# Performance work log

Hardware: AMD Instinct MI355X
Metric: run time of the kernel (lower is better)

## Reference

```python
import jax, jax.numpy as jnp
import numpy as np

D = 128          # embed_dim
N = 400000       # rows in each source state buffer (h_bot/c_bot and h_buf/c_buf)
K = 200000       # gathers per source per child side (M = 2*K merge targets)


def setup_inputs() -> dict:
    key = jax.random.key(0)
    ks = jax.random.split(key, 10)
    h_bot = jax.random.normal(ks[0], (N, D), dtype=jnp.float32)
    c_bot = jax.random.normal(ks[1], (N, D), dtype=jnp.float32)
    h_buf = jax.random.normal(ks[2], (N, D), dtype=jnp.float32)
    c_buf = jax.random.normal(ks[3], (N, D), dtype=jnp.float32)
    bot_from_l = jax.random.randint(ks[4], (K,), 0, N, dtype=jnp.int32)
    prev_from_l = jax.random.randint(ks[5], (K,), 0, N, dtype=jnp.int32)
    bot_from_r = jax.random.randint(ks[6], (K,), 0, N, dtype=jnp.int32)
    prev_from_r = jax.random.randint(ks[7], (K,), 0, N, dtype=jnp.int32)
    # BinaryTreeLSTMCell params: 5 gates (i, o, u, f_l, f_r) over [h_l; h_r]
    W = jax.random.normal(ks[8], (2 * D, 5 * D), dtype=jnp.float32) * (1.0 / np.sqrt(2 * D))
    b = jnp.zeros((5 * D,), dtype=jnp.float32)
    return {"h_bot": h_bot, "c_bot": c_bot, "h_buf": h_buf, "c_buf": c_buf,
            "bot_from_l": bot_from_l, "prev_from_l": prev_from_l,
            "bot_from_r": bot_from_r, "prev_from_r": prev_from_r,
            "W": W, "b": b}


def _multi_select(bot_src, prev_src, bot_from, prev_from):
    # multi_index_select with 'to' ids in concat order: gather rows from the two
    # source buffers into the [M, D] merge-target buffer.
    return jnp.concatenate([bot_src[bot_from], prev_src[prev_from]], axis=0)


def _binary_tree_lstm_cell(h_l, c_l, h_r, c_r, W, b):
    # N-ary (N=2) TreeLSTM merge cell, no input x.
    gates = jnp.concatenate([h_l, h_r], axis=1) @ W + b  # [M, 5D]
    i, o, u, f_l, f_r = jnp.split(gates, 5, axis=1)
    c = jax.nn.sigmoid(i) * jnp.tanh(u) \
        + jax.nn.sigmoid(f_l) * c_l + jax.nn.sigmoid(f_r) * c_r
    h = jax.nn.sigmoid(o) * jnp.tanh(c)
    return h, c


def reference(h_bot, c_bot, h_buf, c_buf,
              bot_from_l, prev_from_l, bot_from_r, prev_from_r, W, b):
    # batch_tree_lstm2: tree_state_select gathers for left and right children,
    # then one BinaryTreeLSTMCell merge over all M targets.
    h_l = _multi_select(h_bot, h_buf, bot_from_l, prev_from_l)
    c_l = _multi_select(c_bot, c_buf, bot_from_l, prev_from_l)
    h_r = _multi_select(h_bot, h_buf, bot_from_r, prev_from_r)
    c_r = _multi_select(c_bot, c_buf, bot_from_r, prev_from_r)
    h, c = _binary_tree_lstm_cell(h_l, c_l, h_r, c_r, W, b)
    return jnp.stack([h, c])  # [2, M, D]
```

## Files before the change

### kernel.cpp

```cpp
#include <hip/hip_runtime.h>

typedef __attribute__((ext_vector_type(8))) short short8_t;
typedef __attribute__((ext_vector_type(4))) float f32x4_t;

#define DDIM 128
#define BM   32
#define LDA  264

__device__ __forceinline__ unsigned short f2bf(float x) {
  union { float f; unsigned u; } v; v.f = x;
  unsigned r = v.u + 0x7FFFu + ((v.u >> 16) & 1u);
  return (unsigned short)(r >> 16);
}

__device__ __forceinline__ float sigf(float x) {
  return __builtin_amdgcn_rcpf(1.0f + __expf(-x));
}
__device__ __forceinline__ float tanh_fast(float x) {
  return 2.0f * __builtin_amdgcn_rcpf(1.0f + __expf(-2.0f * x)) - 1.0f;
}

__global__ void convert_w_kernel(const float* __restrict__ W,
                                 unsigned short* __restrict__ Wt,
                                 int twoD, int fiveD) {
  const int c = blockIdx.x;
  const int k = threadIdx.x;
  Wt[c * twoD + k] = f2bf(W[k * fiveD + c]);
}

__global__ __launch_bounds__(256, 4)
void treelstm_fused_kernel(const float* __restrict__ h_bot,
                           const float* __restrict__ c_bot,
                           const float* __restrict__ h_buf,
                           const float* __restrict__ c_buf,
                           const int* __restrict__ idx_bl,
                           const int* __restrict__ idx_pl,
                           const int* __restrict__ idx_br,
                           const int* __restrict__ idx_pr,
                           const float* __restrict__ bias,
                           const unsigned short* __restrict__ Wt,
                           float* __restrict__ out,
                           int K, int M) {
  __shared__ __align__(16) unsigned short A_lds[BM * LDA];

  const int tid   = threadIdx.x;
  const int mbase = blockIdx.x * BM;

  const int wave = tid >> 6;
  const int lane = tid & 63;
  const int l16  = lane & 15;
  const int lq   = lane >> 4;

  int il[2], ir[2];
  #pragma unroll
  for (int mt = 0; mt < 2; ++mt) {
    int m = mbase + mt * 16 + l16; if (m >= M) m = M - 1;
    il[mt] = (m < K) ? idx_bl[m] : idx_pl[m - K];
    ir[mt] = (m < K) ? idx_br[m] : idx_pr[m - K];
  }

  {
    const int r    = tid >> 3;
    const int seg  = tid & 7;
    const int half = seg >> 2;
    const int cs   = seg & 3;
    int ms = mbase + r; if (ms >= M) ms = M - 1;

    int hidx; const float* hsrc;
    if (half == 0) {
      if (ms < K) { hidx = idx_bl[ms];     hsrc = h_bot; }
      else        { hidx = idx_pl[ms - K]; hsrc = h_buf; }
    } else {
      if (ms < K) { hidx = idx_br[ms];     hsrc = h_bot; }
      else        { hidx = idx_pr[ms - K]; hsrc = h_buf; }
    }
    const float4* s4 = (const float4*)(hsrc + (size_t)hidx * DDIM);
    unsigned short* dst = &A_lds[r * LDA + half * DDIM];
    #pragma unroll
    for (int q = 0; q < 8; ++q) {
      const int f4i = cs + 4 * q;
      float4 v = s4[f4i];
      ushort4 u;
      u.x = f2bf(v.x); u.y = f2bf(v.y); u.z = f2bf(v.z); u.w = f2bf(v.w);
      *(ushort4*)(dst + f4i * 4) = u;
    }
  }
  __syncthreads();

  float* const out_h = out;
  float* const out_c = out + (size_t)M * DDIM;

  const int d0a = wave * 16 + lq * 4;
  const int d0b = d0a + 64;
  f32x4_t cl0[2], cr0[2], cl1[2], cr1[2];
  #pragma unroll
  for (int mt = 0; mt < 2; ++mt) {
    const int m = mbase + mt * 16 + l16;
    const float* cb = (m < K) ? c_bot : c_buf;
    const float* pl = cb + (size_t)il[mt] * DDIM;
    const float* pr = cb + (size_t)ir[mt] * DDIM;
    cl0[mt] = *(const f32x4_t*)(pl + d0a);
    cr0[mt] = *(const f32x4_t*)(pr + d0a);
    cl1[mt] = *(const f32x4_t*)(pl + d0b);
    cr1[mt] = *(const f32x4_t*)(pr + d0b);
  }

#define GEMM_PASS(DBLK, D0, CL, CR)                                          \
  {                                                                          \
    f32x4_t acc[2][5];                                                       \
    _Pragma("unroll")                                                        \
    for (int mt = 0; mt < 2; ++mt)                                           \
      _Pragma("unroll")                                                      \
      for (int g = 0; g < 5; ++g) {                                          \
        f32x4_t z = {0.0f, 0.0f, 0.0f, 0.0f};                                \
        acc[mt][g] = z;                                                      \
      }                                                                      \
    const unsigned short* wb = Wt + (size_t)((DBLK) * 16 + l16) * 256 + lq * 8; \
    const int ab = l16 * LDA + lq * 8;                                       \
    _Pragma("unroll")                                                        \
    for (int kk = 0; kk < 8; ++kk) {                                         \
      const int k0 = kk * 32;                                                \
      short8_t hf[2];                                                        \
      _Pragma("unroll")                                                      \
      for (int mt = 0; mt < 2; ++mt)                                         \
        hf[mt] = *(const short8_t*)(&A_lds[ab + mt * (16 * LDA) + k0]);      \
      _Pragma("unroll")                                                      \
      for (int g = 0; g < 5; ++g) {                                          \
        const short8_t wf =                                                  \
            *(const short8_t*)(wb + (size_t)g * (128 * 256) + k0);           \
        _Pragma("unroll")                                                    \
        for (int mt = 0; mt < 2; ++mt)                                       \
          acc[mt][g] = __builtin_amdgcn_mfma_f32_16x16x32_bf16(              \
              wf, hf[mt], acc[mt][g], 0, 0, 0);                              \
      }                                                                      \
    }                                                                        \
    f32x4_t bs[5];                                                           \
    _Pragma("unroll")                                                        \
    for (int g = 0; g < 5; ++g)                                              \
      bs[g] = *(const f32x4_t*)(bias + g * DDIM + (D0));                     \
    _Pragma("unroll")                                                        \
    for (int mt = 0; mt < 2; ++mt) {                                         \
      const int m = mbase + mt * 16 + l16;                                   \
      if (m < M) {                                                           \
        f32x4_t hv4, cv4;                                                    \
        _Pragma("unroll")                                                    \
        for (int j = 0; j < 4; ++j) {                                        \
          const float gi = acc[mt][0][j] + bs[0][j];                         \
          const float go = acc[mt][1][j] + bs[1][j];                         \
          const float gu = acc[mt][2][j] + bs[2][j];                         \
          const float gl = acc[mt][3][j] + bs[3][j];                         \
          const float gr = acc[mt][4][j] + bs[4][j];                         \
          const float cn = sigf(gi) * tanh_fast(gu)                          \
                         + sigf(gl) * CL[mt][j] + sigf(gr) * CR[mt][j];      \
          const float hn = sigf(go) * tanh_fast(cn);                         \
          cv4[j] = cn; hv4[j] = hn;                                          \
        }                                                                    \
        const size_t off = (size_t)m * DDIM + (D0);                          \
        __builtin_nontemporal_store(hv4, (f32x4_t*)(out_h + off));           \
        __builtin_nontemporal_store(cv4, (f32x4_t*)(out_c + off));           \
      }                                                                      \
    }                                                                        \
  }

  GEMM_PASS(wave,     d0a, cl0, cr0)
  GEMM_PASS(wave + 4, d0b, cl1, cr1)
#undef GEMM_PASS
}

extern "C" void kernel_launch(void* const* d_in, const int* in_sizes, int n_in,
                              void* d_out, int out_size, void* d_ws, size_t ws_size,
                              hipStream_t stream) {
  const float* h_bot  = (const float*)d_in[0];
  const float* c_bot  = (const float*)d_in[1];
  const float* h_buf  = (const float*)d_in[2];
  const float* c_buf  = (const float*)d_in[3];
  const int*   idx_bl = (const int*)d_in[4];
  const int*   idx_pl = (const int*)d_in[5];
  const int*   idx_br = (const int*)d_in[6];
  const int*   idx_pr = (const int*)d_in[7];
  const float* W      = (const float*)d_in[8];
  const float* bias   = (const float*)d_in[9];

  const int K = in_sizes[4];
  const int M = 2 * K;
  const int fiveD = in_sizes[9];
  const int twoD  = in_sizes[8] / fiveD;

  unsigned short* Wt = (unsigned short*)d_ws;

  hipLaunchKernelGGL(convert_w_kernel, dim3(fiveD), dim3(twoD), 0, stream,
                     W, Wt, twoD, fiveD);

  const int grid = (M + BM - 1) / BM;
  hipLaunchKernelGGL(treelstm_fused_kernel, dim3(grid), dim3(256), 0, stream,
                     h_bot, c_bot, h_buf, c_buf,
                     idx_bl, idx_pl, idx_br, idx_pr,
                     bias, Wt, (float*)d_out, K, M);
}
```

Before: 628.7 us.

## Make treelstm kernel persistent with double-buffered LDS gather prefetch

Converts the one-tile-per-block kernel into a persistent kernel with a capped grid of 1024 blocks that loop over tiles. The h-row gather for the next tile is issued into registers before the current tile's GEMM and written to a second LDS buffer, overlapping gather latency with MFMA work. The c-state gathers move to just before each GEMM pass, and output stores switch from nontemporal to plain stores. This adds register pressure from the prefetched float4s and doubles LDS use, which may reduce occupancy, and the capped grid may leave the GPU underfilled when gather latency dominates.

Result: slower. 1.476 ms (+134.8%).

```diff
diff --git a/kernel.cpp b/kernel.cpp
--- a/kernel.cpp
+++ b/kernel.cpp
@@ -6,6 +6,7 @@
 #define DDIM 128
 #define BM   32
 #define LDA  264
+#define NBLK 1024
 
 __device__ __forceinline__ unsigned short f2bf(float x) {
   union { float f; unsigned u; } v; v.f = x;
@@ -40,72 +41,67 @@
                            const float* __restrict__ bias,
                            const unsigned short* __restrict__ Wt,
                            float* __restrict__ out,
-                           int K, int M) {
-  __shared__ __align__(16) unsigned short A_lds[BM * LDA];
-
-  const int tid   = threadIdx.x;
-  const int mbase = blockIdx.x * BM;
-
+                           int K, int M, int ntiles) {
+  __shared__ __align__(16) unsigned short A_lds[2][BM * LDA];
+
+  const int tid  = threadIdx.x;
   const int wave = tid >> 6;
   const int lane = tid & 63;
   const int l16  = lane & 15;
   const int lq   = lane >> 4;
-
-  int il[2], ir[2];
-  #pragma unroll
-  for (int mt = 0; mt < 2; ++mt) {
-    int m = mbase + mt * 16 + l16; if (m >= M) m = M - 1;
-    il[mt] = (m < K) ? idx_bl[m] : idx_pl[m - K];
-    ir[mt] = (m < K) ? idx_br[m] : idx_pr[m - K];
-  }
-
-  {
-    const int r    = tid >> 3;
-    const int seg  = tid & 7;
-    const int half = seg >> 2;
-    const int cs   = seg & 3;
-    int ms = mbase + r; if (ms >= M) ms = M - 1;
-
-    int hidx; const float* hsrc;
-    if (half == 0) {
-      if (ms < K) { hidx = idx_bl[ms];     hsrc = h_bot; }
-      else        { hidx = idx_pl[ms - K]; hsrc = h_buf; }
-    } else {
-      if (ms < K) { hidx = idx_br[ms];     hsrc = h_bot; }
-      else        { hidx = idx_pr[ms - K]; hsrc = h_buf; }
-    }
-    const float4* s4 = (const float4*)(hsrc + (size_t)hidx * DDIM);
-    unsigned short* dst = &A_lds[r * LDA + half * DDIM];
-    #pragma unroll
-    for (int q = 0; q < 8; ++q) {
-      const int f4i = cs + 4 * q;
-      float4 v = s4[f4i];
-      ushort4 u;
-      u.x = f2bf(v.x); u.y = f2bf(v.y); u.z = f2bf(v.z); u.w = f2bf(v.w);
-      *(ushort4*)(dst + f4i * 4) = u;
-    }
-  }
-  __syncthreads();
+  const int d0a  = wave * 16 + lq * 4;
+  const int d0b  = d0a + 64;
+
+  const int sr    = tid >> 3;
+  const int seg   = tid & 7;
+  const int shalf = seg >> 2;
+  const int scs   = seg & 3;
 
   float* const out_h = out;
   float* const out_c = out + (size_t)M * DDIM;
 
-  const int d0a = wave * 16 + lq * 4;
-  const int d0b = d0a + 64;
-  f32x4_t cl0[2], cr0[2], cl1[2], cr1[2];
-  #pragma unroll
-  for (int mt = 0; mt < 2; ++mt) {
-    const int m = mbase + mt * 16 + l16;
-    const float* cb = (m < K) ? c_bot : c_buf;
-    const float* pl = cb + (size_t)il[mt] * DDIM;
-    const float* pr = cb + (size_t)ir[mt] * DDIM;
-    cl0[mt] = *(const f32x4_t*)(pl + d0a);
-    cr0[mt] = *(const f32x4_t*)(pr + d0a);
-    cl1[mt] = *(const f32x4_t*)(pl + d0b);
-    cr1[mt] = *(const f32x4_t*)(pr + d0b);
-  }
-
-#define GEMM_PASS(DBLK, D0, CL, CR)                                          \
+  const int step = gridDim.x;
+  int t = blockIdx.x;
+  if (t >= ntiles) return;
+
+#define SIDX(tt, dst)                                                        \
+  { int m = (tt) * BM + sr; if (m >= M) m = M - 1;                           \
+    if (shalf == 0) dst = (m < K) ? idx_bl[m] : idx_pl[m - K];               \
+    else            dst = (m < K) ? idx_br[m] : idx_pr[m - K]; }
+
+#define EPI_IDX(tt, dl, dr)                                                  \
+  { _Pragma("unroll")                                                        \
+    for (int mt = 0; mt < 2; ++mt) {                                         \
+      int m = (tt) * BM + mt * 16 + l16; if (m >= M) m = M - 1;              \
+      dl[mt] = (m < K) ? idx_bl[m] : idx_pl[m - K];                          \
+      dr[mt] = (m < K) ? idx_br[m] : idx_pr[m - K]; } }
+
+#define H_GATHER(tt, sidx, hv)                                               \
+  { int m = (tt) * BM + sr; if (m >= M) m = M - 1;                           \
+    const float* hb = (m < K) ? h_bot : h_buf;                               \
+    const float4* s4 = (const float4*)(hb + (size_t)(sidx) * DDIM);          \
+    _Pragma("unroll")                                                        \
+    for (int q = 0; q < 8; ++q) hv[q] = s4[scs + 4 * q]; }
+
+#define H_WRITE(bufp, hv)                                                    \
+  { unsigned short* dst = &(bufp)[sr * LDA + shalf * DDIM];                  \
+    _Pragma("unroll")                                                        \
+    for (int q = 0; q < 8; ++q) {                                            \
+      const int f4i = scs + 4 * q;                                           \
+      ushort4 u;                                                             \
+      u.x = f2bf(hv[q].x); u.y = f2bf(hv[q].y);                              \
+      u.z = f2bf(hv[q].z); u.w = f2bf(hv[q].w);                              \
+      *(ushort4*)(dst + f4i * 4) = u; } }
+
+#define C_GATHER(tt, dl, dr, D0, cl, cr)                                     \
+  { _Pragma("unroll")                                                        \
+    for (int mt = 0; mt < 2; ++mt) {                                         \
+      int m = (tt) * BM + mt * 16 + l16; if (m >= M) m = M - 1;              \
+      const float* cb = (m < K) ? c_bot : c_buf;                             \
+      cl[mt] = *(const f32x4_t*)(cb + (size_t)dl[mt] * DDIM + (D0));         \
+      cr[mt] = *(const f32x4_t*)(cb + (size_t)dr[mt] * DDIM + (D0)); } }
+
+#define GEMM_PASS(bufp, DBLK, D0, CL, CR)                                    \
   {                                                                          \
     f32x4_t acc[2][5];                                                       \
     _Pragma("unroll")                                                        \
@@ -123,7 +119,7 @@
       short8_t hf[2];                                                        \
       _Pragma("unroll")                                                      \
       for (int mt = 0; mt < 2; ++mt)                                         \
-        hf[mt] = *(const short8_t*)(&A_lds[ab + mt * (16 * LDA) + k0]);      \
+        hf[mt] = *(const short8_t*)(&(bufp)[ab + mt * (16 * LDA) + k0]);     \
       _Pragma("unroll")                                                      \
       for (int g = 0; g < 5; ++g) {                                          \
         const short8_t wf =                                                  \
@@ -140,7 +136,7 @@
       bs[g] = *(const f32x4_t*)(bias + g * DDIM + (D0));                     \
     _Pragma("unroll")                                                        \
     for (int mt = 0; mt < 2; ++mt) {                                         \
-      const int m = mbase + mt * 16 + l16;                                   \
+      const int m = t * BM + mt * 16 + l16;                                  \
       if (m < M) {                                                           \
         f32x4_t hv4, cv4;                                                    \
         _Pragma("unroll")                                                    \
@@ -155,15 +151,64 @@
           const float hn = sigf(go) * tanh_fast(cn);                         \
           cv4[j] = cn; hv4[j] = hn;                                          \
         }                                                                    \
-        const size_t off = (size_t)m * DDIM + (D0);                          \
-        __builtin_nontemporal_store(hv4, (f32x4_t*)(out_h + off));           \
-        __builtin_nontemporal_store(cv4, (f32x4_t*)(out_c + off));           \
+        const size_t off = (size_t)m * DDIM + (D0);                         \
+        *(f32x4_t*)(out_h + off) = hv4;                                      \
+        *(f32x4_t*)(out_c + off) = cv4;                                      \
       }                                                                      \
     }                                                                        \
   }
 
-  GEMM_PASS(wave,     d0a, cl0, cr0)
-  GEMM_PASS(wave + 4, d0b, cl1, cr1)
+  int il[2], ir[2];
+  EPI_IDX(t, il, ir);
+  {
+    int s0; SIDX(t, s0);
+    float4 hv0[8];
+    H_GATHER(t, s0, hv0);
+    H_WRITE(A_lds[0], hv0);
+  }
+  int sidx_n = 0;
+  if (t + step < ntiles) SIDX(t + step, sidx_n);
+  __syncthreads();
+
+  int cur = 0;
+  for (;;) {
+    const int tn = t + step;
+    const bool more = (tn < ntiles);
+    unsigned short* const bufc = A_lds[cur];
+    unsigned short* const bufn = A_lds[cur ^ 1];
+
+    float4 hv[8];
+    if (more) H_GATHER(tn, sidx_n, hv);
+
+    f32x4_t cl0[2], cr0[2];
+    C_GATHER(t, il, ir, d0a, cl0, cr0);
+
+    int sidx_n2 = 0;
+    int il_n[2], ir_n[2];
+    if (tn + step < ntiles) SIDX(tn + step, sidx_n2);
+    if (more) EPI_IDX(tn, il_n, ir_n);
+
+    GEMM_PASS(bufc, wave, d0a, cl0, cr0);
+
+    if (more) H_WRITE(bufn, hv);
+
+    f32x4_t cl1[2], cr1[2];
+    C_GATHER(t, il, ir, d0b, cl1, cr1);
+    GEMM_PASS(bufc, wave + 4, d0b, cl1, cr1);
+
+    if (!more) break;
+    sidx_n = sidx_n2;
+    il[0] = il_n[0]; il[1] = il_n[1];
+    ir[0] = ir_n[0]; ir[1] = ir_n[1];
+    t = tn;
+    __syncthreads();
+    cur ^= 1;
+  }
+#undef SIDX
+#undef EPI_IDX
+#undef H_GATHER
+#undef H_WRITE
+#undef C_GATHER
 #undef GEMM_PASS
 }
 
@@ -191,9 +236,10 @@
   hipLaunchKernelGGL(convert_w_kernel, dim3(fiveD), dim3(twoD), 0, stream,
                      W, Wt, twoD, fiveD);
 
-  const int grid = (M + BM - 1) / BM;
+  const int ntiles = (M + BM - 1) / BM;
+  const int grid = (ntiles < NBLK) ? ntiles : NBLK;
   hipLaunchKernelGGL(treelstm_fused_kernel, dim3(grid), dim3(256), 0, stream,
                      h_bot, c_bot, h_buf, c_buf,
                      idx_bl, idx_pl, idx_br, idx_pr,
-                     bias, Wt, (float*)d_out, K, M);
-}
+                     bias, Wt, (float*)d_out, K, M, ntiles);
+}
```
